# Kernel optimization log

Measured on AMD Instinct MI355X. Metric: run time of the kernel, lower is better.

Reference implementation:

```python
import jax, jax.numpy as jnp
import numpy as np

B, S, N, D = 1, 512, 384, 64
H, DP, DQK = 32, 128, 64
LAMBDA_INIT = 1.0
EPS = 1e-32
SCALING = DQK ** -0.5


def _layer_norm(x, g, b):
    m = jnp.mean(x, axis=-1, keepdims=True)
    v = jnp.mean(jnp.square(x - m), axis=-1, keepdims=True)
    return (x - m) * jax.lax.rsqrt(v + 1e-5) * g + b


def setup_inputs() -> dict:
    key = jax.random.key(0)
    ks = jax.random.split(key, 12)
    msa = jax.random.normal(ks[0], (B, S, N, D), dtype=jnp.float32)
    Wq = jax.random.normal(ks[1], (2 * DQK, D), dtype=jnp.float32) * 0.02
    Wk = Wq + jax.random.normal(ks[2], (2 * DQK, D), dtype=jnp.float32) * 0.1 * 0.02
    Wl = jax.random.normal(ks[3], (H, D), dtype=jnp.float32) * 0.02
    Wr = jax.random.normal(ks[4], (H, D), dtype=jnp.float32) * 0.02
    Wp = jax.random.normal(ks[5], (2 * DP, H * H), dtype=jnp.float32) * 0.02
    bp = jnp.zeros((2 * DP,), dtype=jnp.float32)
    lq1 = jax.random.normal(ks[6], (DQK,), dtype=jnp.float32) * 0.1
    lk1 = jax.random.normal(ks[7], (DQK,), dtype=jnp.float32) * 0.1
    lq2 = jax.random.normal(ks[8], (DQK,), dtype=jnp.float32) * 0.1
    lk2 = jax.random.normal(ks[9], (DQK,), dtype=jnp.float32) * 0.1
    return {
        'msa': msa,
        'ln_g': jnp.ones((D,), jnp.float32), 'ln_b': jnp.zeros((D,), jnp.float32),
        'Wq': Wq, 'Wk': Wk,
        'qn_g': jnp.ones((DQK,), jnp.float32), 'qn_b': jnp.zeros((DQK,), jnp.float32),
        'kn_g': jnp.ones((DQK,), jnp.float32), 'kn_b': jnp.zeros((DQK,), jnp.float32),
        'lq1': lq1, 'lk1': lk1, 'lq2': lq2, 'lk2': lk2,
        'Wl': Wl, 'Wr': Wr, 'Wp': Wp, 'bp': bp,
    }


def reference(msa, ln_g, ln_b, Wq, Wk, qn_g, qn_b, kn_g, kn_b,
              lq1, lk1, lq2, lk2, Wl, Wr, Wp, bp):
    b, s, n, d = msa.shape
    x = _layer_norm(msa, ln_g, ln_b)  # [b,s,n,d]

    # differential sequence attention (all masks are all-True by default)
    q = (x[:, 0] @ Wq.T).reshape(b, n, 2, DQK).transpose(0, 2, 1, 3)       # [b,2,n,dqk]
    k = (x @ Wk.T).reshape(b, s, n, 2, DQK).transpose(0, 3, 1, 2, 4)       # [b,2,s,n,dqk]
    q = _layer_norm(q, qn_g, qn_b)
    k = _layer_norm(k, kn_g, kn_b)
    sw = jnp.einsum('btnd,btsnd->btsn', q, k) * SCALING                     # [b,2,s,n]
    sw = sw.sum(axis=-1) / (n + EPS)                                        # [b,2,s]
    lam = jnp.exp(jnp.sum(lq1 * lk1)) - jnp.exp(jnp.sum(lq2 * lk2)) + LAMBDA_INIT
    sw = sw[:, 0] - lam * sw[:, 1]                                          # [b,s]
    seq_weights = jax.nn.softmax(sw, axis=-1)                               # [b,s]

    # weighted left/right hidden projections
    a = jnp.einsum('bsnd,hd->bnsh', x, Wl)
    bt = jnp.einsum('bsnd,hd->bnsh', x, Wr)
    ws = jnp.sqrt(seq_weights + EPS)[:, None, :, None]                      # [b,1,s,1]
    a = a * ws
    bt = bt * ws

    # outer product mean over sequences, then pairwise projection + SwiGLU
    outer = jnp.einsum('bisc,bjse->bijce', a, bt).reshape(b, n, n, H * H)   # [b,n,n,h^2]
    out = outer @ Wp.T + bp                                                 # [b,n,n,2*dp]
    val, gate = jnp.split(out, 2, axis=-1)
    return jax.nn.silu(gate) * val                                          # [b,n,n,dp]
```

## Files before the change

### kernel.cpp

```cpp
#include <hip/hip_runtime.h>
#include <hip/hip_bf16.h>
#include <math.h>

#define WS_X        0u
#define WS_AEXT     12582912u
#define WS_BEXT     18874368u
#define WS_QG       25165824u
#define WS_SQG      25214976u
#define WS_SQB      25215744u
#define WS_PART     25216512u
#define WS_WSQ      25219584u
#define WS_BPP      25220096u
#define WS_WPF      25220352u

typedef __attribute__((ext_vector_type(8))) short bf16x8;
typedef __attribute__((ext_vector_type(4))) float f32x4;

union U4B8 { uint4 u4; unsigned u[4]; bf16x8 v; };

__device__ __forceinline__ unsigned short f2b(float x) {
    __hip_bfloat16 b = __float2bfloat16(x);
    return *reinterpret_cast<unsigned short*>(&b);
}
__device__ __forceinline__ float b2f(unsigned short u) {
    __hip_bfloat16 b = *reinterpret_cast<__hip_bfloat16*>(&u);
    return __bfloat162float(b);
}

#define GLDS(g, l) __builtin_amdgcn_global_load_lds(                                   \
    (const __attribute__((address_space(1))) unsigned int*)(g),                        \
    (__attribute__((address_space(3))) unsigned int*)(l), 16, 0, 0)

__global__ __launch_bounds__(256) void k1_ln(const float* __restrict__ msa,
                                             const float* __restrict__ g,
                                             const float* __restrict__ bb,
                                             float* __restrict__ x) {
    int row = blockIdx.x * 16 + (threadIdx.x >> 4);
    int l16 = threadIdx.x & 15;
    float4 v = ((const float4*)msa)[(size_t)row * 16 + l16];
    float sum = v.x + v.y + v.z + v.w;
    #pragma unroll
    for (int m = 1; m < 16; m <<= 1) sum += __shfl_xor(sum, m);
    float mean = sum * (1.0f / 64.0f);
    float4 dv = make_float4(v.x - mean, v.y - mean, v.z - mean, v.w - mean);
    float sq = dv.x * dv.x + dv.y * dv.y + dv.z * dv.z + dv.w * dv.w;
    #pragma unroll
    for (int m = 1; m < 16; m <<= 1) sq += __shfl_xor(sq, m);
    float r = rsqrtf(sq * (1.0f / 64.0f) + 1e-5f);
    float4 g4 = ((const float4*)g)[l16];
    float4 b4 = ((const float4*)bb)[l16];
    ((float4*)x)[(size_t)row * 16 + l16] = make_float4(
        dv.x * r * g4.x + b4.x, dv.y * r * g4.y + b4.y,
        dv.z * r * g4.z + b4.z, dv.w * r * g4.w + b4.w);
}

__global__ __launch_bounds__(128) void k2_q(const float* __restrict__ x,
                                            const float* __restrict__ Wq,
                                            const float* __restrict__ qg_,
                                            const float* __restrict__ qb_,
                                            const float* __restrict__ kg_,
                                            const float* __restrict__ kb_,
                                            float* __restrict__ qgOut,
                                            float* __restrict__ SqgOut,
                                            float* __restrict__ SqbOut) {
    int n = blockIdx.x;
    int tt = threadIdx.x >> 6;
    int d = threadIdx.x & 63;
    const float* xr = x + (size_t)n * 64;
    const float* w  = Wq + (size_t)(tt * 64 + d) * 64;
    float acc = 0.f;
    #pragma unroll 8
    for (int dd = 0; dd < 64; ++dd) acc += xr[dd] * w[dd];
    float sum = acc;
    #pragma unroll
    for (int m = 1; m < 64; m <<= 1) sum += __shfl_xor(sum, m);
    float mean = sum * (1.0f / 64.0f);
    float dv = acc - mean;
    float sq = dv * dv;
    #pragma unroll
    for (int m = 1; m < 64; m <<= 1) sq += __shfl_xor(sq, m);
    float r = rsqrtf(sq * (1.0f / 64.0f) + 1e-5f);
    float qnv = dv * r * qg_[d] + qb_[d];
    float qgv = qnv * kg_[d];
    float sb  = qnv * kb_[d];
    float sg  = qgv;
    #pragma unroll
    for (int m = 1; m < 64; m <<= 1) { sg += __shfl_xor(sg, m); sb += __shfl_xor(sb, m); }
    qgOut[(size_t)(tt * 384 + n) * 64 + d] = qgv;
    if (d == 0) { SqgOut[tt * 384 + n] = sg; SqbOut[tt * 384 + n] = sb; }
}

__global__ __launch_bounds__(256) void gemm_k3(const float* __restrict__ X,
                                               const float* __restrict__ Wk,
                                               const float* __restrict__ qg,
                                               const float* __restrict__ Sqg,
                                               const float* __restrict__ Sqb,
                                               float* __restrict__ part) {
    __shared__ __align__(16) char smem[65536];
    float (*AsT)[132] = (float(*)[132])smem;
    float (*BsT)[132] = (float(*)[132])(smem + 16896);
    float* kbuf = (float*)smem;

    int t  = threadIdx.x;
    int m0 = blockIdx.x * 128;
    int s  = m0 / 384;
    int nchunk = (m0 - s * 384) >> 7;
    int tr = t >> 4, tc = t & 15;
    float acc[8][8] = {};
    int rrow = t >> 3;
    int kk   = (t & 7) * 4;
    for (int k0 = 0; k0 < 64; k0 += 32) {
        #pragma unroll
        for (int l = 0; l < 4; ++l) {
            int row = rrow + 32 * l;
            float4 va = *(const float4*)(X + (size_t)(m0 + row) * 64 + k0 + kk);
            AsT[kk + 0][row] = va.x; AsT[kk + 1][row] = va.y;
            AsT[kk + 2][row] = va.z; AsT[kk + 3][row] = va.w;
            float4 vb = *(const float4*)(Wk + (size_t)row * 64 + k0 + kk);
            BsT[kk + 0][row] = vb.x; BsT[kk + 1][row] = vb.y;
            BsT[kk + 2][row] = vb.z; BsT[kk + 3][row] = vb.w;
        }
        __syncthreads();
        #pragma unroll 4
        for (int k = 0; k < 32; ++k) {
            float a[8], b[8];
            *(float4*)&a[0] = *(const float4*)&AsT[k][tr * 8];
            *(float4*)&a[4] = *(const float4*)&AsT[k][tr * 8 + 4];
            *(float4*)&b[0] = *(const float4*)&BsT[k][tc * 8];
            *(float4*)&b[4] = *(const float4*)&BsT[k][tc * 8 + 4];
            #pragma unroll
            for (int q = 0; q < 8; ++q)
                #pragma unroll
                for (int j = 0; j < 8; ++j)
                    acc[q][j] += a[q] * b[j];
        }
        __syncthreads();
    }
    #pragma unroll
    for (int q = 0; q < 8; ++q) {
        int m = tr * 8 + q;
        int swz = (m & 15) << 4;
        int b0 = m * 512 + (((tc * 2) * 16) ^ swz);
        int b1 = m * 512 + (((tc * 2 + 1) * 16) ^ swz);
        *(float4*)((char*)kbuf + b0) = make_float4(acc[q][0], acc[q][1], acc[q][2], acc[q][3]);
        *(float4*)((char*)kbuf + b1) = make_float4(acc[q][4], acc[q][5], acc[q][6], acc[q][7]);
    }
    __syncthreads();
    int r  = t & 127;
    int tt = t >> 7;
    int n  = nchunk * 128 + r;
    const char* base = (const char*)kbuf + r * 512;
    const float4* qgp = (const float4*)(qg + ((size_t)(tt * 384 + n)) * 64);
    int swz = (r & 15) << 4;
    float s1 = 0.f, s2 = 0.f, s3 = 0.f;
    #pragma unroll
    for (int i = 0; i < 16; ++i) {
        float4 kv = *(const float4*)(base + ((((tt * 16 + i) * 16) ^ swz)));
        float4 qv = qgp[i];
        s1 += kv.x + kv.y + kv.z + kv.w;
        s2 += kv.x * kv.x + kv.y * kv.y + kv.z * kv.z + kv.w * kv.w;
        s3 += kv.x * qv.x + kv.y * qv.y + kv.z * qv.z + kv.w * qv.w;
    }
    float mu  = s1 * (1.0f / 64.0f);
    float var = s2 * (1.0f / 64.0f) - mu * mu;
    float rln = rsqrtf(var + 1e-5f);
    float dot = rln * (s3 - mu * Sqg[tt * 384 + n]) + Sqb[tt * 384 + n];
    #pragma unroll
    for (int m = 1; m < 64; m <<= 1) dot += __shfl_xor(dot, m);
    __syncthreads();
    if ((t & 63) == 0) kbuf[t >> 6] = dot;
    __syncthreads();
    if (t == 0) part[((size_t)0 * 512 + s) * 3 + nchunk] = kbuf[0] + kbuf[1];
    if (t == 1) part[((size_t)1 * 512 + s) * 3 + nchunk] = kbuf[2] + kbuf[3];
}

__global__ __launch_bounds__(512) void k4_softmax(const float* __restrict__ part,
                                                  const float* __restrict__ lq1,
                                                  const float* __restrict__ lk1,
                                                  const float* __restrict__ lq2,
                                                  const float* __restrict__ lk2,
                                                  float* __restrict__ wsq) {
    int s = threadIdx.x;
    float l1 = 0.f, l2 = 0.f;
    for (int i = 0; i < 64; ++i) { l1 += lq1[i] * lk1[i]; l2 += lq2[i] * lk2[i]; }
    float lam = expf(l1) - expf(l2) + 1.0f;
    const float c = 0.125f / 384.0f;
    float a0 = (part[s * 3] + part[s * 3 + 1] + part[s * 3 + 2]) * c;
    float a1 = (part[(512 + s) * 3] + part[(512 + s) * 3 + 1] + part[(512 + s) * 3 + 2]) * c;
    float v = a0 - lam * a1;
    __shared__ float red[512];
    red[s] = v;
    __syncthreads();
    for (int off = 256; off > 0; off >>= 1) {
        if (s < off) red[s] = fmaxf(red[s], red[s + off]);
        __syncthreads();
    }
    float mx = red[0];
    __syncthreads();
    float e = expf(v - mx);
    red[s] = e;
    __syncthreads();
    for (int off = 256; off > 0; off >>= 1) {
        if (s < off) red[s] += red[s + off];
        __syncthreads();
    }
    wsq[s] = sqrtf(e / red[0] + 1e-32f);
}

__global__ __launch_bounds__(256) void k5_ab(const float* __restrict__ x,
                                             const float* __restrict__ Wl,
                                             const float* __restrict__ Wr,
                                             const float* __restrict__ wsq,
                                             unsigned short* __restrict__ AHo,
                                             unsigned short* __restrict__ ALo,
                                             unsigned short* __restrict__ BHo,
                                             unsigned short* __restrict__ BLo) {
    int i  = blockIdx.x;
    int s0 = blockIdx.y * 64;
    int t  = threadIdx.x;
    __shared__ __align__(16) float wl[2048], wr[2048];
    __shared__ float xT[64][69];
    ((float4*)wl)[t * 2]     = ((const float4*)Wl)[t * 2];
    ((float4*)wl)[t * 2 + 1] = ((const float4*)Wl)[t * 2 + 1];
    ((float4*)wr)[t * 2]     = ((const float4*)Wr)[t * 2];
    ((float4*)wr)[t * 2 + 1] = ((const float4*)Wr)[t * 2 + 1];
    {
        int s_l = t >> 2, d0 = (t & 3) * 16;
        const float* xr = x + ((size_t)(s0 + s_l) * 384 + i) * 64 + d0;
        #pragma unroll
        for (int j = 0; j < 4; ++j) {
            float4 v = *(const float4*)(xr + j * 4);
            xT[d0 + j * 4 + 0][s_l] = v.x; xT[d0 + j * 4 + 1][s_l] = v.y;
            xT[d0 + j * 4 + 2][s_l] = v.z; xT[d0 + j * 4 + 3][s_l] = v.w;
        }
    }
    __syncthreads();
    int c = t >> 3, so = (t & 7) * 8;
    float aa[8] = {}, bb2[8] = {};
    #pragma unroll 8
    for (int d = 0; d < 64; ++d) {
        float wlv = wl[c * 64 + d], wrv = wr[c * 64 + d];
        #pragma unroll
        for (int q = 0; q < 8; ++q) {
            float xv = xT[d][so + q];
            aa[q]  += xv * wlv;
            bb2[q] += xv * wrv;
        }
    }
    #pragma unroll
    for (int q = 0; q < 8; ++q) {
        float wq = wsq[s0 + so + q];
        aa[q] *= wq; bb2[q] *= wq;
    }
    int m = i * 32 + c;
    int s = s0 + so;
    size_t idx = (((size_t)(m >> 4) * 16 + (s >> 5)) * 64 + ((m & 15) | (((s >> 3) & 3) << 4))) * 8;
    {
        unsigned short h[8], l[8];
        #pragma unroll
        for (int q = 0; q < 8; ++q) { h[q] = f2b(aa[q]); l[q] = f2b(aa[q] - b2f(h[q])); }
        *(uint4*)&AHo[idx] = make_uint4((unsigned)h[0] | ((unsigned)h[1] << 16), (unsigned)h[2] | ((unsigned)h[3] << 16),
                                        (unsigned)h[4] | ((unsigned)h[5] << 16), (unsigned)h[6] | ((unsigned)h[7] << 16));
        *(uint4*)&ALo[idx] = make_uint4((unsigned)l[0] | ((unsigned)l[1] << 16), (unsigned)l[2] | ((unsigned)l[3] << 16),
                                        (unsigned)l[4] | ((unsigned)l[5] << 16), (unsigned)l[6] | ((unsigned)l[7] << 16));
    }
    {
        unsigned short h[8], l[8];
        #pragma unroll
        for (int q = 0; q < 8; ++q) { h[q] = f2b(bb2[q]); l[q] = f2b(bb2[q] - b2f(h[q])); }
        *(uint4*)&BHo[idx] = make_uint4((unsigned)h[0] | ((unsigned)h[1] << 16), (unsigned)h[2] | ((unsigned)h[3] << 16),
                                        (unsigned)h[4] | ((unsigned)h[5] << 16), (unsigned)h[6] | ((unsigned)h[7] << 16));
        *(uint4*)&BLo[idx] = make_uint4((unsigned)l[0] | ((unsigned)l[1] << 16), (unsigned)l[2] | ((unsigned)l[3] << 16),
                                        (unsigned)l[4] | ((unsigned)l[5] << 16), (unsigned)l[6] | ((unsigned)l[7] << 16));
    }
}

__global__ __launch_bounds__(256) void prep_wp(const float* __restrict__ Wp,
                                               const float* __restrict__ bp,
                                               unsigned short* __restrict__ WpF,
                                               float* __restrict__ bpP) {
    int gid = blockIdx.x * 256 + threadIdx.x;
    int lane  = gid & 63;
    int kstep = (gid >> 6) & 31;
    int nb    = (gid >> 11) & 15;
    int bsel  = gid >> 15;
    int rl = lane & 15, kg = lane >> 4;
    int urow = nb * 16 + rl;
    int srow = (urow & 1) ? 128 + (urow >> 1) : (urow >> 1);
    int k0 = kstep * 32 + kg * 8;
    const float* src = Wp + (size_t)srow * 1024 + k0;
    unsigned short o[8];
    #pragma unroll
    for (int e = 0; e < 8; ++e) {
        float w = src[e];
        unsigned short h = f2b(w);
        o[e] = bsel ? f2b(w - b2f(h)) : h;
    }
    *(uint4*)&WpF[(size_t)gid * 8] = make_uint4(
        (unsigned)o[0] | ((unsigned)o[1] << 16), (unsigned)o[2] | ((unsigned)o[3] << 16),
        (unsigned)o[4] | ((unsigned)o[5] << 16), (unsigned)o[6] | ((unsigned)o[7] << 16));
    if (blockIdx.x == 0) {
        int tt = threadIdx.x;
        bpP[tt] = bp[(tt & 1) ? 128 + (tt >> 1) : (tt >> 1)];
    }
}

__global__ __launch_bounds__(256) void gemm_fused(const unsigned short* __restrict__ AH,
                                                  const unsigned short* __restrict__ AL,
                                                  const unsigned short* __restrict__ BHm,
                                                  const unsigned short* __restrict__ BLm,
                                                  const unsigned short* __restrict__ WpF,
                                                  const float* __restrict__ bpP,
                                                  float* __restrict__ out) {
    __shared__ __align__(16) unsigned char smem[65536];
    unsigned* pa = (unsigned*)smem;

    const int t = threadIdx.x;
    const int wave = t >> 6, lane = t & 63;
    const int bx = blockIdx.x, by = blockIdx.y;
    const int m0 = bx * 128, n0 = by * 128;
    const int wm = (wave & 1) * 64, wn = (wave >> 1) * 64;
    const int kgrp = lane >> 4, rl = lane & 15;
    f32x4 acc[4][4] = {};

    const unsigned short* srcArr = (wave == 0) ? AH : (wave == 1) ? AL : (wave == 2) ? BHm : BLm;
    const unsigned short* srcBase = srcArr + ((size_t)(((wave < 2) ? m0 : n0) >> 4) * 16) * 512 + lane * 8;
    unsigned short* dstW = (unsigned short*)smem + wave * 4096;

    #pragma unroll
    for (int pane = 0; pane < 8; ++pane)
        GLDS(srcBase + (size_t)pane * 8192, dstW + pane * 512);
    __syncthreads();

    #pragma unroll 2
    for (int kt = 0; kt < 16; ++kt) {
        if (kt < 15) {
            unsigned short* dst = dstW + ((kt + 1) & 1) * 16384;
            const unsigned short* s2 = srcBase + (size_t)(kt + 1) * 512;
            #pragma unroll
            for (int pane = 0; pane < 8; ++pane)
                GLDS(s2 + (size_t)pane * 8192, dst + pane * 512);
        }
        const int cb = (kt & 1) * 32768;
        bf16x8 aHf[4], aLf[4], bHf[4], bLf[4];
        #pragma unroll
        for (int f = 0; f < 4; ++f) {
            const int pA = ((wm >> 4) + f) * 1024;
            aHf[f] = *(const bf16x8*)(smem + cb + pA + lane * 16);
            aLf[f] = *(const bf16x8*)(smem + cb + 8192 + pA + lane * 16);
            const int pB = ((wn >> 4) + f) * 1024;
            bHf[f] = *(const bf16x8*)(smem + cb + 16384 + pB + lane * 16);
            bLf[f] = *(const bf16x8*)(smem + cb + 24576 + pB + lane * 16);
        }
        __builtin_amdgcn_s_setprio(1);
        #pragma unroll
        for (int mf = 0; mf < 4; ++mf)
            #pragma unroll
            for (int nf = 0; nf < 4; ++nf) {
                acc[mf][nf] = __builtin_amdgcn_mfma_f32_16x16x32_bf16(aHf[mf], bHf[nf], acc[mf][nf], 0, 0, 0);
                acc[mf][nf] = __builtin_amdgcn_mfma_f32_16x16x32_bf16(aLf[mf], bHf[nf], acc[mf][nf], 0, 0, 0);
                acc[mf][nf] = __builtin_amdgcn_mfma_f32_16x16x32_bf16(aHf[mf], bLf[nf], acc[mf][nf], 0, 0, 0);
            }
        __builtin_amdgcn_s_setprio(0);
        __syncthreads();
    }

    #pragma unroll
    for (int mf = 0; mf < 4; ++mf) {
        #pragma unroll
        for (int nf = 0; nf < 4; ++nf) {
            #pragma unroll
            for (int r = 0; r < 4; ++r) {
                int mloc = wm + mf * 16 + kgrp * 4 + r;
                int nloc = wn + nf * 16 + rl;
                int p = ((mloc >> 5) << 2) | (nloc >> 5);
                int k = ((mloc & 31) << 5) | (nloc & 31);
                float v = acc[mf][nf][r];
                unsigned short h = f2b(v);
                unsigned short l = f2b(v - b2f(h));
                pa[(p << 10) + (k ^ ((p & 3) << 3))] = (unsigned)h | ((unsigned)l << 16);
            }
        }
    }
    __syncthreads();

    f32x4 acc2[4] = {};
    const unsigned* paRow = pa + (rl << 10);
    const int kg8 = kgrp * 8;
    #pragma unroll 4
    for (int ks = 0; ks < 32; ++ks) {
        U4B8 ua0, ua1, aHf, aLf;
        int kb = (ks * 32 + kg8) ^ ((rl & 3) << 3);
        ua0.u4 = *(const uint4*)(paRow + kb);
        ua1.u4 = *(const uint4*)(paRow + kb + 4);
        aHf.u[0] = __builtin_amdgcn_perm(ua0.u[1], ua0.u[0], 0x05040100u);
        aHf.u[1] = __builtin_amdgcn_perm(ua0.u[3], ua0.u[2], 0x05040100u);
        aHf.u[2] = __builtin_amdgcn_perm(ua1.u[1], ua1.u[0], 0x05040100u);
        aHf.u[3] = __builtin_amdgcn_perm(ua1.u[3], ua1.u[2], 0x05040100u);
        aLf.u[0] = __builtin_amdgcn_perm(ua0.u[1], ua0.u[0], 0x07060302u);
        aLf.u[1] = __builtin_amdgcn_perm(ua0.u[3], ua0.u[2], 0x07060302u);
        aLf.u[2] = __builtin_amdgcn_perm(ua1.u[1], ua1.u[0], 0x07060302u);
        aLf.u[3] = __builtin_amdgcn_perm(ua1.u[3], ua1.u[2], 0x07060302u);
        bf16x8 bHf[4], bLf[4];
        #pragma unroll
        for (int nf = 0; nf < 4; ++nf) {
            const int nb = wave * 4 + nf;
            bHf[nf] = *(const bf16x8*)&WpF[(size_t)((nb * 32 + ks) * 64 + lane) * 8];
            bLf[nf] = *(const bf16x8*)&WpF[(size_t)(((16 + nb) * 32 + ks) * 64 + lane) * 8];
        }
        __builtin_amdgcn_s_setprio(1);
        #pragma unroll
        for (int nf = 0; nf < 4; ++nf) {
            acc2[nf] = __builtin_amdgcn_mfma_f32_16x16x32_bf16(aHf.v, bHf[nf], acc2[nf], 0, 0, 0);
            acc2[nf] = __builtin_amdgcn_mfma_f32_16x16x32_bf16(aLf.v, bHf[nf], acc2[nf], 0, 0, 0);
            acc2[nf] = __builtin_amdgcn_mfma_f32_16x16x32_bf16(aHf.v, bLf[nf], acc2[nf], 0, 0, 0);
        }
        __builtin_amdgcn_s_setprio(0);
    }

    const int parity = rl & 1;
    #pragma unroll
    for (int nf = 0; nf < 4; ++nf) {
        const int np = wave * 64 + nf * 16 + rl;
        const float bias = bpP[np];
        const int ocol = np >> 1;
        #pragma unroll
        for (int r = 0; r < 4; ++r) {
            float own = acc2[nf][r] + bias;
            float oth = __shfl_xor(own, 1);
            float v = parity ? oth : own;
            float g = parity ? own : oth;
            float res = v * (g / (1.0f + expf(-g)));
            if (parity == (r >> 1)) {
                int p = kgrp * 4 + r;
                int i = bx * 4 + (p >> 2);
                int j = by * 4 + (p & 3);
                out[((size_t)i * 384 + j) * 128 + ocol] = res;
            }
        }
    }
}

extern "C" void kernel_launch(void* const* d_in, const int* in_sizes, int n_in,
                              void* d_out, int out_size, void* d_ws, size_t ws_size,
                              hipStream_t stream) {
    const float* msa  = (const float*)d_in[0];
    const float* ln_g = (const float*)d_in[1];
    const float* ln_b = (const float*)d_in[2];
    const float* Wq   = (const float*)d_in[3];
    const float* Wk   = (const float*)d_in[4];
    const float* qn_g = (const float*)d_in[5];
    const float* qn_b = (const float*)d_in[6];
    const float* kn_g = (const float*)d_in[7];
    const float* kn_b = (const float*)d_in[8];
    const float* lq1  = (const float*)d_in[9];
    const float* lk1  = (const float*)d_in[10];
    const float* lq2  = (const float*)d_in[11];
    const float* lk2  = (const float*)d_in[12];
    const float* Wl   = (const float*)d_in[13];
    const float* Wr   = (const float*)d_in[14];
    const float* Wp   = (const float*)d_in[15];
    const float* bp   = (const float*)d_in[16];
    float* out = (float*)d_out;
    float* ws  = (float*)d_ws;

    float* x = ws + WS_X;
    unsigned short* AHs = (unsigned short*)(ws + WS_AEXT);
    unsigned short* ALs = (unsigned short*)(ws + WS_AEXT + 3145728u);
    unsigned short* BHs = (unsigned short*)(ws + WS_BEXT);
    unsigned short* BLs = (unsigned short*)(ws + WS_BEXT + 3145728u);
    float* qg   = ws + WS_QG;
    float* Sqg  = ws + WS_SQG;
    float* Sqb  = ws + WS_SQB;
    float* part = ws + WS_PART;
    float* wsq  = ws + WS_WSQ;
    float* bpP  = ws + WS_BPP;
    unsigned short* WpF = (unsigned short*)(ws + WS_WPF);

    prep_wp<<<256, 256, 0, stream>>>(Wp, bp, WpF, bpP);
    k1_ln<<<12288, 256, 0, stream>>>(msa, ln_g, ln_b, x);
    k2_q<<<384, 128, 0, stream>>>(x, Wq, qn_g, qn_b, kn_g, kn_b, qg, Sqg, Sqb);
    gemm_k3<<<1536, 256, 0, stream>>>(x, Wk, qg, Sqg, Sqb, part);
    k4_softmax<<<1, 512, 0, stream>>>(part, lq1, lk1, lq2, lk2, wsq);
    k5_ab<<<dim3(384, 8), 256, 0, stream>>>(x, Wl, Wr, wsq, AHs, ALs, BHs, BLs);
    gemm_fused<<<dim3(96, 96), 256, 0, stream>>>(AHs, ALs, BHs, BLs, WpF, bpP, out);
}
```

Before: 848.5 us.

## Load A fragments directly into registers, keep only B tiles in LDS

The GEMM now prefetches each wave's A-operand fragments (hi and lo bf16 halves) from global memory straight into double-buffered registers, and only stages the B tiles through LDS. This halves LDS traffic and footprint per stage and removes the A ds_reads. In exchange, each pair of waves sharing an M half redundantly fetches the same A data from global/L2, and register pressure rises from the doubled A buffers.

```diff
diff --git a/kernel.cpp b/kernel.cpp
--- a/kernel.cpp
+++ b/kernel.cpp
@@ -323,43 +323,53 @@
     const int kgrp = lane >> 4, rl = lane & 15;
     f32x4 acc[4][4] = {};
 
-    const unsigned short* srcArr = (wave == 0) ? AH : (wave == 1) ? AL : (wave == 2) ? BHm : BLm;
-    const unsigned short* srcBase = srcArr + ((size_t)(((wave < 2) ? m0 : n0) >> 4) * 16) * 512 + lane * 8;
-    unsigned short* dstW = (unsigned short*)smem + wave * 4096;
-
-    #pragma unroll
-    for (int pane = 0; pane < 8; ++pane)
-        GLDS(srcBase + (size_t)pane * 8192, dstW + pane * 512);
+    const unsigned short* aHb = AH + (size_t)((m0 + wm) >> 4) * 8192 + lane * 8;
+    const unsigned short* aLb = AL + (size_t)((m0 + wm) >> 4) * 8192 + lane * 8;
+    const unsigned short* bArr = (wave < 2) ? BHm : BLm;
+    const unsigned short* bSrc = bArr + (size_t)((n0 >> 4) + (wave & 1) * 4) * 8192 + lane * 8;
+    const int dstOffB = (wave >> 1) * 8192 + (wave & 1) * 4096;
+
+    bf16x8 aHr[2][4], aLr[2][4];
+    #pragma unroll
+    for (int p = 0; p < 4; ++p)
+        GLDS(bSrc + (size_t)p * 8192, (unsigned short*)(smem + dstOffB + p * 1024));
+    #pragma unroll
+    for (int f = 0; f < 4; ++f) {
+        aHr[0][f] = *(const bf16x8*)(aHb + (size_t)f * 8192);
+        aLr[0][f] = *(const bf16x8*)(aLb + (size_t)f * 8192);
+    }
     __syncthreads();
 
     #pragma unroll 2
     for (int kt = 0; kt < 16; ++kt) {
+        const int cur = kt & 1, nxt = cur ^ 1;
         if (kt < 15) {
-            unsigned short* dst = dstW + ((kt + 1) & 1) * 16384;
-            const unsigned short* s2 = srcBase + (size_t)(kt + 1) * 512;
+            const unsigned short* s2 = bSrc + (size_t)(kt + 1) * 512;
             #pragma unroll
-            for (int pane = 0; pane < 8; ++pane)
-                GLDS(s2 + (size_t)pane * 8192, dst + pane * 512);
-        }
-        const int cb = (kt & 1) * 32768;
-        bf16x8 aHf[4], aLf[4], bHf[4], bLf[4];
+            for (int p = 0; p < 4; ++p)
+                GLDS(s2 + (size_t)p * 8192, (unsigned short*)(smem + nxt * 16384 + dstOffB + p * 1024));
+            #pragma unroll
+            for (int f = 0; f < 4; ++f) {
+                aHr[nxt][f] = *(const bf16x8*)(aHb + (size_t)f * 8192 + (kt + 1) * 512);
+                aLr[nxt][f] = *(const bf16x8*)(aLb + (size_t)f * 8192 + (kt + 1) * 512);
+            }
+        }
+        const int cb = cur * 16384;
+        bf16x8 bHf[4], bLf[4];
         #pragma unroll
         for (int f = 0; f < 4; ++f) {
-            const int pA = ((wm >> 4) + f) * 1024;
-            aHf[f] = *(const bf16x8*)(smem + cb + pA + lane * 16);
-            aLf[f] = *(const bf16x8*)(smem + cb + 8192 + pA + lane * 16);
             const int pB = ((wn >> 4) + f) * 1024;
-            bHf[f] = *(const bf16x8*)(smem + cb + 16384 + pB + lane * 16);
-            bLf[f] = *(const bf16x8*)(smem + cb + 24576 + pB + lane * 16);
+            bHf[f] = *(const bf16x8*)(smem + cb + pB + lane * 16);
+            bLf[f] = *(const bf16x8*)(smem + cb + 8192 + pB + lane * 16);
         }
         __builtin_amdgcn_s_setprio(1);
         #pragma unroll
         for (int mf = 0; mf < 4; ++mf)
             #pragma unroll
             for (int nf = 0; nf < 4; ++nf) {
-                acc[mf][nf] = __builtin_amdgcn_mfma_f32_16x16x32_bf16(aHf[mf], bHf[nf], acc[mf][nf], 0, 0, 0);
-                acc[mf][nf] = __builtin_amdgcn_mfma_f32_16x16x32_bf16(aLf[mf], bHf[nf], acc[mf][nf], 0, 0, 0);
-                acc[mf][nf] = __builtin_amdgcn_mfma_f32_16x16x32_bf16(aHf[mf], bLf[nf], acc[mf][nf], 0, 0, 0);
+                acc[mf][nf] = __builtin_amdgcn_mfma_f32_16x16x32_bf16(aHr[cur][mf], bHf[nf], acc[mf][nf], 0, 0, 0);
+                acc[mf][nf] = __builtin_amdgcn_mfma_f32_16x16x32_bf16(aLr[cur][mf], bHf[nf], acc[mf][nf], 0, 0, 0);
+                acc[mf][nf] = __builtin_amdgcn_mfma_f32_16x16x32_bf16(aHr[cur][mf], bLf[nf], acc[mf][nf], 0, 0, 0);
             }
         __builtin_amdgcn_s_setprio(0);
         __syncthreads();
```

After: 858.9 us. No clear change (+1.2%).
